# Optimization experiments

Hardware: AMD Instinct MI355X
Metric: run time of the kernel (lower is better)

Reference implementation:

```python
import jax, jax.numpy as jnp
import numpy as np

B = 256      # graphs per batch
N = 512      # nodes per graph
FEAT = 64    # num_features
H = 64       # nhid
DEG = 16     # avg degree
RATIO = 0.5  # pooling_ratio
E = B * N * DEG


def setup_inputs() -> dict:
    key = jax.random.key(0)
    ks = jax.random.split(key, 12)
    # edges constructed within each graph via offsets
    src_loc = jax.random.randint(ks[0], (B, N * DEG), 0, N)
    dst_loc = jax.random.randint(ks[1], (B, N * DEG), 0, N)
    offs = (jnp.arange(B) * N)[:, None]
    edge_src = (src_loc + offs).reshape(-1).astype(jnp.int32)
    edge_dst = (dst_loc + offs).reshape(-1).astype(jnp.int32)
    batch = jnp.repeat(jnp.arange(B, dtype=jnp.int32), N)
    x = jax.random.normal(ks[2], (B * N, FEAT), dtype=jnp.float32)
    edge_attr = jax.random.uniform(ks[3], (E,), dtype=jnp.float32) + 0.1
    s1 = 1.0 / np.sqrt(FEAT)
    s2 = 1.0 / np.sqrt(H)
    return {
        "x": x,
        "edge_attr": edge_attr,
        "W1": jax.random.normal(ks[4], (FEAT, H), jnp.float32) * s1,
        "b1": jnp.zeros((H,), jnp.float32),
        "Wp1": jax.random.normal(ks[5], (H, 1), jnp.float32) * s2,
        "bp1": jnp.zeros((1,), jnp.float32),
        "W2": jax.random.normal(ks[6], (H, H), jnp.float32) * s2,
        "b2": jnp.zeros((H,), jnp.float32),
        "Wp2": jax.random.normal(ks[7], (H, 1), jnp.float32) * s2,
        "bp2": jnp.zeros((1,), jnp.float32),
        "edge_src": edge_src,
        "edge_dst": edge_dst,
        "batch": batch,
    }


def gcn_conv(x, W, b, src, dst, ew, n):
    """PyG GCNConv: sym-normalized weighted adjacency + self-loops (weight 1)."""
    h = x @ W                                   # [n, out]
    deg = jnp.zeros((n,), x.dtype).at[dst].add(ew) + 1.0  # self-loop adds 1
    dinv = jax.lax.rsqrt(deg)
    coef = dinv[dst] * ew * dinv[src]           # [E]
    out = jnp.zeros_like(h).at[dst].add(coef[:, None] * h[src])
    out = out + h * (1.0 / deg)[:, None]        # self-loop term: deg^-0.5 * 1 * deg^-0.5
    return out + b


def sag_pool(x, src, dst, ew, Wp, bp, n_per):
    """SAGPool: score = GCNConv(x)->1, per-graph top-k, gate by tanh(score),
    filter edges (dropped edges represented by zero weight)."""
    n = x.shape[0]
    score = gcn_conv(x, Wp, bp, src, dst, ew, n)[:, 0]   # [n]
    k = int(np.ceil(RATIO * n_per))
    _, idx = jax.lax.top_k(score.reshape(B, n_per), k)   # [B, k] local indices
    perm = (idx + (jnp.arange(B) * n_per)[:, None]).reshape(-1)
    xn = x[perm] * jnp.tanh(score[perm])[:, None]        # [B*k, H]
    newid = jnp.full((n,), -1, jnp.int32).at[perm].set(
        jnp.arange(B * k, dtype=jnp.int32))
    ns, nd = newid[src], newid[dst]
    valid = (ns >= 0) & (nd >= 0)
    ew2 = jnp.where(valid, ew, 0.0)
    ns = jnp.where(valid, ns, 0)
    nd = jnp.where(valid, nd, 0)
    return xn, ns, nd, ew2, k


def readout(x, k):
    """[gmp || gap] per graph; each graph has exactly k nodes, contiguous."""
    xg = x.reshape(B, k, -1)
    return jnp.concatenate([xg.max(axis=1), xg.mean(axis=1)], axis=1)  # [B, 2H]


def reference(x, edge_attr, W1, b1, Wp1, bp1, W2, b2, Wp2, bp2,
              edge_src, edge_dst, batch):
    n0 = x.shape[0]
    h = jax.nn.relu(gcn_conv(x, W1, b1, edge_src, edge_dst, edge_attr, n0))
    h, s1, d1, w1e, k1 = sag_pool(h, edge_src, edge_dst, edge_attr, Wp1, bp1, N)
    x1 = readout(h, k1)
    h = jax.nn.relu(gcn_conv(h, W2, b2, s1, d1, w1e, B * k1))
    h, _, _, _, k2 = sag_pool(h, s1, d1, w1e, Wp2, bp2, k1)
    x2 = readout(h, k2)
    return (x1 + x2) / 2.0
```

## Files before the change

kernel.cpp:

```cpp
#include <hip/hip_runtime.h>
#include <math.h>

#define BG   256
#define NN   512
#define EPG  (NN * 16)
#define NE   (BG * EPG)
#define N0   (BG * NN)
#define K1   256
#define N1_  (BG * K1)
#define K2   128
#define N2_  (BG * K2)

__device__ __forceinline__ float4 f4fma(float s, float4 a, float4 c) {
    c.x = fmaf(s, a.x, c.x); c.y = fmaf(s, a.y, c.y);
    c.z = fmaf(s, a.z, c.z); c.w = fmaf(s, a.w, c.w);
    return c;
}

template <int NPG, bool REMAP>
__global__ __launch_bounds__(512)
void stage_head_kernel(const int* __restrict__ esrc, const int* __restrict__ edst,
                       const float* __restrict__ eatt, const int* __restrict__ nid,
                       int2* __restrict__ pairs, int* __restrict__ rowstart,
                       int* __restrict__ rowcnt, float* __restrict__ dinv,
                       const float4* __restrict__ X4, const float4* __restrict__ W4,
                       float4* __restrict__ Y4, int nrows, int mmb) {
    __shared__ __align__(16) char smem[52224];
    if ((int)blockIdx.x < BG) {
        int2*  lpair = (int2*)smem;
        int*   cnt   = (int*)(smem + 32768);
        float* wsum  = (float*)(smem + 32768) + NPG;
        int*   scn   = (int*)(smem + 32768) + 2 * NPG;
        float* sdinv = (float*)(smem + 32768) + 3 * NPG;
        int*   wtot  = (int*)(smem + 32768) + 4 * NPG;
        int g = blockIdx.x;
        int e0 = g * EPG, nbase = g * NPG;
        for (int ii = threadIdx.x; ii < NPG; ii += 512) { cnt[ii] = 0; wsum[ii] = 0.f; }
        __syncthreads();
        const int4*   edst4 = (const int4*)(edst + e0);
        const int4*   esrc4 = (const int4*)(esrc + e0);
        const float4* eatt4 = (const float4*)(eatt + e0);
        int ed[16]; int es[16]; float ea[16];
#pragma unroll
        for (int c = 0; c < 4; ++c) {
            int ch = threadIdx.x + c * 512;
            int4   dd = edst4[ch];
            int4   ss = esrc4[ch];
            float4 ww = eatt4[ch];
            ed[c * 4 + 0] = dd.x; ed[c * 4 + 1] = dd.y; ed[c * 4 + 2] = dd.z; ed[c * 4 + 3] = dd.w;
            es[c * 4 + 0] = ss.x; es[c * 4 + 1] = ss.y; es[c * 4 + 2] = ss.z; es[c * 4 + 3] = ss.w;
            ea[c * 4 + 0] = ww.x; ea[c * 4 + 1] = ww.y; ea[c * 4 + 2] = ww.z; ea[c * 4 + 3] = ww.w;
        }
        if (REMAP) {
#pragma unroll
            for (int j = 0; j < 16; ++j) { ed[j] = nid[ed[j]]; es[j] = nid[es[j]]; }
        }
#pragma unroll
        for (int j = 0; j < 16; ++j) {
            bool valid = !REMAP || (ed[j] >= 0 && es[j] >= 0);
            if (valid) {
                int dl = ed[j] - nbase;
                atomicAdd(&cnt[dl], 1);
                atomicAdd(&wsum[dl], ea[j]);
            }
        }
        __syncthreads();
        int i = threadIdx.x;
        int lane = i & 63, wvid = i >> 6;
        int xval = (i < NPG) ? cnt[i] : 0;
        int xs = xval;
#pragma unroll
        for (int off = 1; off < 64; off <<= 1) {
            int v = __shfl_up(xs, off, 64);
            if (lane >= off) xs += v;
        }
        if (lane == 63) wtot[wvid] = xs;
        __syncthreads();
        int woff = 0, total = 0;
#pragma unroll
        for (int t = 0; t < 8; ++t) {
            int wt = wtot[t];
            if (t < wvid) woff += wt;
            total += wt;
        }
        xs += woff;
        if (i < NPG) {
            int st = xs - xval;
            rowstart[nbase + i] = e0 + st;
            rowcnt[nbase + i]   = xval;
            float di = rsqrtf(wsum[i] + 1.0f);
            dinv[nbase + i] = di;
            sdinv[i] = di;
            scn[i] = st;
        }
        __syncthreads();
        int slots[16]; float cf[16];
#pragma unroll
        for (int j = 0; j < 16; ++j) {
            bool valid = !REMAP || (ed[j] >= 0 && es[j] >= 0);
            slots[j] = -1;
            if (valid) {
                int dl = ed[j] - nbase, sl = es[j] - nbase;
                cf[j] = sdinv[dl] * ea[j] * sdinv[sl];
                slots[j] = atomicAdd(&scn[dl], 1);
            }
        }
#pragma unroll
        for (int j = 0; j < 16; ++j)
            if (slots[j] >= 0 && slots[j] < 4096)
                lpair[slots[j]] = make_int2(es[j], __float_as_int(cf[j]));
        __syncthreads();
        int n0 = total < 4096 ? total : 4096;
        for (int k = threadIdx.x; k < n0; k += 512) pairs[e0 + k] = lpair[k];
        __syncthreads();
        if (total > 4096) {
#pragma unroll
            for (int j = 0; j < 16; ++j)
                if (slots[j] >= 4096)
                    lpair[slots[j] - 4096] = make_int2(es[j], __float_as_int(cf[j]));
            __syncthreads();
            int n1 = total - 4096;
            for (int k = threadIdx.x; k < n1; k += 512) pairs[e0 + 4096 + k] = lpair[k];
        }
    } else {
        float (*sW)[68] = (float (*)[68])smem;
        int p = threadIdx.x >> 8;
        int t = threadIdx.x & 255;
        float (*sX)[68] = (float (*)[68])(smem + 17408 + p * 17408);
#pragma unroll
        for (int u = 0; u < 2; ++u) {
            int idx = threadIdx.x + u * 512;
            int r = idx >> 4, c4 = idx & 15;
            *(float4*)&sW[r][c4 * 4] = W4[idx];
        }
        int mb = blockIdx.x - BG;
        int ntiles = nrows >> 6;
        int rg = t >> 4, cg = t & 15;
        for (int tile = mb * 2 + p; tile < ntiles; tile += mmb * 2) {
            __syncthreads();
            int row0 = tile << 6;
#pragma unroll
            for (int u = 0; u < 4; ++u) {
                int idx = t + u * 256;
                int r = idx >> 4, c4 = idx & 15;
                *(float4*)&sX[r][c4 * 4] = X4[(size_t)(row0 + r) * 16 + c4];
            }
            __syncthreads();
            float4 acc0 = make_float4(0.f, 0.f, 0.f, 0.f);
            float4 acc1 = acc0, acc2 = acc0, acc3 = acc0;
#pragma unroll
            for (int k4 = 0; k4 < 16; ++k4) {
                float4 xv0 = *(const float4*)&sX[rg * 4 + 0][k4 * 4];
                float4 xv1 = *(const float4*)&sX[rg * 4 + 1][k4 * 4];
                float4 xv2 = *(const float4*)&sX[rg * 4 + 2][k4 * 4];
                float4 xv3 = *(const float4*)&sX[rg * 4 + 3][k4 * 4];
                float4 wv0 = *(const float4*)&sW[k4 * 4 + 0][cg * 4];
                float4 wv1 = *(const float4*)&sW[k4 * 4 + 1][cg * 4];
                float4 wv2 = *(const float4*)&sW[k4 * 4 + 2][cg * 4];
                float4 wv3 = *(const float4*)&sW[k4 * 4 + 3][cg * 4];
                acc0 = f4fma(xv0.x, wv0, acc0); acc0 = f4fma(xv0.y, wv1, acc0);
                acc0 = f4fma(xv0.z, wv2, acc0); acc0 = f4fma(xv0.w, wv3, acc0);
                acc1 = f4fma(xv1.x, wv0, acc1); acc1 = f4fma(xv1.y, wv1, acc1);
                acc1 = f4fma(xv1.z, wv2, acc1); acc1 = f4fma(xv1.w, wv3, acc1);
                acc2 = f4fma(xv2.x, wv0, acc2); acc2 = f4fma(xv2.y, wv1, acc2);
                acc2 = f4fma(xv2.z, wv2, acc2); acc2 = f4fma(xv2.w, wv3, acc2);
                acc3 = f4fma(xv3.x, wv0, acc3); acc3 = f4fma(xv3.y, wv1, acc3);
                acc3 = f4fma(xv3.z, wv2, acc3); acc3 = f4fma(xv3.w, wv3, acc3);
            }
            size_t ob = (size_t)(row0 + rg * 4) * 16 + cg;
            Y4[ob]      = acc0;
            Y4[ob + 16] = acc1;
            Y4[ob + 32] = acc2;
            Y4[ob + 48] = acc3;
        }
    }
}

template <int NPG, int K, bool FINAL>
__global__ __launch_bounds__(512)
void tail_kernel(const float4* __restrict__ hx4, const int2* __restrict__ pairs,
                 const int* __restrict__ rowstart, const int* __restrict__ rowcnt,
                 const float* __restrict__ dinv, const float4* __restrict__ b4,
                 const float4* __restrict__ wp4, const float* __restrict__ bp,
                 int* __restrict__ nid, float4* __restrict__ xn4,
                 float* __restrict__ xr, const float* __restrict__ x1r,
                 float* __restrict__ out) {
    constexpr int PASSES = NPG / 32;
    __shared__ __align__(16) char smem[NPG * 68 * 4];
    float* shx = (float*)smem;
    float* shp = (float*)smem;
    float* ssc = (float*)smem + NPG;
    int*   rnk = (int*)smem + 2 * NPG;
    float4* smx = (float4*)(smem + 3 * NPG * 4);
    float4* ssm = smx + 32 * 16;

    int g = blockIdx.x, nbase = g * NPG;
    int t = threadIdx.x;
    int lane16 = t & 15, sub = (t >> 4) & 3, wv = t >> 6;
    for (int i = t; i < NPG * 16; i += 512) {
        int r = i >> 4, c4 = i & 15;
        *(float4*)&shx[r * 68 + c4 * 4] = hx4[(size_t)nbase * 16 + i];
    }
    __syncthreads();
    float4 acc[PASSES];
    float  hpreg[PASSES];
    float4 bb = b4[lane16];
    float4 w4 = wp4[lane16];
#pragma unroll
    for (int p = 0; p < PASSES; ++p) {
        int nl = p * 32 + wv * 4 + sub;
        int node = nbase + nl;
        float di = dinv[node];
        int st = rowstart[node], cn = rowcnt[node];
        float dii = di * di;
        float4 a = *(const float4*)&shx[nl * 68 + lane16 * 4];
        a.x = fmaf(a.x, dii, bb.x);
        a.y = fmaf(a.y, dii, bb.y);
        a.z = fmaf(a.z, dii, bb.z);
        a.w = fmaf(a.w, dii, bb.w);
        for (int j = 0; j < cn; ++j) {
            int2 pr = pairs[st + j];
            const float4 v = *(const float4*)&shx[(pr.x - nbase) * 68 + lane16 * 4];
            a = f4fma(__int_as_float(pr.y), v, a);
        }
        a.x = fmaxf(a.x, 0.f); a.y = fmaxf(a.y, 0.f);
        a.z = fmaxf(a.z, 0.f); a.w = fmaxf(a.w, 0.f);
        acc[p] = a;
        float tt = a.x * w4.x + a.y * w4.y + a.z * w4.z + a.w * w4.w;
        tt += __shfl_xor(tt, 1, 64); tt += __shfl_xor(tt, 2, 64);
        tt += __shfl_xor(tt, 4, 64); tt += __shfl_xor(tt, 8, 64);
        hpreg[p] = tt;
    }
    __syncthreads();
#pragma unroll
    for (int p = 0; p < PASSES; ++p) {
        int nl = p * 32 + wv * 4 + sub;
        if (lane16 == 0) shp[nl] = hpreg[p];
    }
    __syncthreads();
    for (int i = t; i < NPG; i += 512) {
        int st = rowstart[nbase + i], cn = rowcnt[nbase + i];
        float di = dinv[nbase + i];
        float a = fmaf(shp[i], di * di, bp[0]);
        for (int j = 0; j < cn; ++j) {
            int2 pr = pairs[st + j];
            a = fmaf(__int_as_float(pr.y), shp[pr.x - nbase], a);
        }
        ssc[i] = a;
    }
    __syncthreads();
    for (int i = t; i < NPG; i += 512) {
        float si = ssc[i];
        int rank = 0;
        for (int j = 0; j < NPG; ++j) {
            float sj = ssc[j];
            rank += (sj > si) || (sj == si && j < i);
        }
        rnk[i] = rank;
        if (!FINAL) nid[nbase + i] = (rank < K) ? (g * K + rank) : -1;
    }
    __syncthreads();
    float4 mx = make_float4(-3.402823466e38f, -3.402823466e38f, -3.402823466e38f, -3.402823466e38f);
    float4 sm = make_float4(0.f, 0.f, 0.f, 0.f);
#pragma unroll
    for (int p = 0; p < PASSES; ++p) {
        int nl = p * 32 + wv * 4 + sub;
        int r = rnk[nl];
        if (r < K) {
            float gt = tanhf(ssc[nl]);
            float4 v = acc[p];
            v.x *= gt; v.y *= gt; v.z *= gt; v.w *= gt;
            if (!FINAL) xn4[((size_t)g * K + r) * 16 + lane16] = v;
            mx.x = fmaxf(mx.x, v.x); mx.y = fmaxf(mx.y, v.y);
            mx.z = fmaxf(mx.z, v.z); mx.w = fmaxf(mx.w, v.w);
            sm.x += v.x; sm.y += v.y; sm.z += v.z; sm.w += v.w;
        }
    }
    int grp = t >> 4;
    smx[grp * 16 + lane16] = mx;
    ssm[grp * 16 + lane16] = sm;
    __syncthreads();
    if (grp == 0) {
#pragma unroll
        for (int u = 1; u < 32; ++u) {
            float4 a = smx[u * 16 + lane16], b = ssm[u * 16 + lane16];
            mx.x = fmaxf(mx.x, a.x); mx.y = fmaxf(mx.y, a.y);
            mx.z = fmaxf(mx.z, a.z); mx.w = fmaxf(mx.w, a.w);
            sm.x += b.x; sm.y += b.y; sm.z += b.z; sm.w += b.w;
        }
        float invK = 1.f / K;
        int c = lane16 * 4;
        float mr[4] = {mx.x, mx.y, mx.z, mx.w};
        float ar[4] = {sm.x * invK, sm.y * invK, sm.z * invK, sm.w * invK};
#pragma unroll
        for (int u = 0; u < 4; ++u) {
            if (FINAL) {
                out[g * 128 + c + u]      = 0.5f * (x1r[g * 128 + c + u]      + mr[u]);
                out[g * 128 + 64 + c + u] = 0.5f * (x1r[g * 128 + 64 + c + u] + ar[u]);
            } else {
                xr[g * 128 + c + u]      = mr[u];
                xr[g * 128 + 64 + c + u] = ar[u];
            }
        }
    }
}

extern "C" void kernel_launch(void* const* d_in, const int* in_sizes, int n_in,
                              void* d_out, int out_size, void* d_ws, size_t ws_size,
                              hipStream_t stream) {
    const float* x    = (const float*)d_in[0];
    const float* eatt = (const float*)d_in[1];
    const float* W1   = (const float*)d_in[2];
    const float* b1   = (const float*)d_in[3];
    const float* Wp1  = (const float*)d_in[4];
    const float* bp1  = (const float*)d_in[5];
    const float* W2   = (const float*)d_in[6];
    const float* b2   = (const float*)d_in[7];
    const float* Wp2  = (const float*)d_in[8];
    const float* bp2  = (const float*)d_in[9];
    const int*   esrc = (const int*)d_in[10];
    const int*   edst = (const int*)d_in[11];
    float* out = (float*)d_out;

    float* ws = (float*)d_ws;
    size_t o = 0;
    float* A    = ws + o; o += (size_t)N0 * 64;
    float* xn1  = ws + o; o += (size_t)N1_ * 64;
    int2*  prs  = (int2*)(ws + o); o += (size_t)NE * 2;
    int*   rst  = (int*)(ws + o); o += N0;
    int*   rcn  = (int*)(ws + o); o += N0;
    float* dinv = ws + o; o += N0;
    int*   nid  = (int*)(ws + o); o += N0;
    float* x1r  = ws + o; o += BG * 128;

    float* hx1 = A;
    float* hx2 = A;

    stage_head_kernel<NN, false><<<BG + 512, 512, 0, stream>>>(
        esrc, edst, eatt, nullptr, prs, rst, rcn, dinv,
        (const float4*)x, (const float4*)W1, (float4*)hx1, N0, 512);
    tail_kernel<NN, K1, false><<<BG, 512, 0, stream>>>(
        (const float4*)hx1, prs, rst, rcn, dinv, (const float4*)b1,
        (const float4*)Wp1, bp1, nid, (float4*)xn1, x1r, nullptr, nullptr);
    stage_head_kernel<K1, true><<<BG + 256, 512, 0, stream>>>(
        esrc, edst, eatt, nid, prs, rst, rcn, dinv,
        (const float4*)xn1, (const float4*)W2, (float4*)hx2, N1_, 256);
    tail_kernel<K1, K2, true><<<BG, 512, 0, stream>>>(
        (const float4*)hx2, prs, rst, rcn, dinv, (const float4*)b2,
        (const float4*)Wp2, bp2, nullptr, nullptr, nullptr, x1r, out);
}
```

Measured before the change: 247.2 us.

## Sort nodes by degree and aggregate full feature rows per thread in tail

The tail kernel now buckets nodes by in-degree with a shared-memory histogram and prefix scan, then assigns one node per thread so each thread accumulates all 64 features for its row. The aim is to cut wavefront divergence from uneven neighbour counts and to reuse each loaded pair across 16 float4s, with a one-ahead prefetch of the next pair. Pair sources are stored as graph-local indices so the subtraction of nbase is dropped in the inner loops. In exchange it uses 64 accumulator registers per thread, more shared memory and extra barriers, and leaves half the threads idle when NPG is 256; the per-thread row reads from shared memory may also cause bank conflicts.

```diff
diff --git a/kernel.cpp b/kernel.cpp
--- a/kernel.cpp
+++ b/kernel.cpp
@@ -108,7 +108,7 @@
 #pragma unroll
         for (int j = 0; j < 16; ++j)
             if (slots[j] >= 0 && slots[j] < 4096)
-                lpair[slots[j]] = make_int2(es[j], __float_as_int(cf[j]));
+                lpair[slots[j]] = make_int2(es[j] - nbase, __float_as_int(cf[j]));
         __syncthreads();
         int n0 = total < 4096 ? total : 4096;
         for (int k = threadIdx.x; k < n0; k += 512) pairs[e0 + k] = lpair[k];
@@ -117,7 +117,7 @@
 #pragma unroll
             for (int j = 0; j < 16; ++j)
                 if (slots[j] >= 4096)
-                    lpair[slots[j] - 4096] = make_int2(es[j], __float_as_int(cf[j]));
+                    lpair[slots[j] - 4096] = make_int2(es[j] - nbase, __float_as_int(cf[j]));
             __syncthreads();
             int n1 = total - 4096;
             for (int k = threadIdx.x; k < n1; k += 512) pairs[e0 + 4096 + k] = lpair[k];
@@ -186,65 +186,107 @@
                  float* __restrict__ xr, const float* __restrict__ x1r,
                  float* __restrict__ out) {
     constexpr int PASSES = NPG / 32;
-    __shared__ __align__(16) char smem[NPG * 68 * 4];
-    float* shx = (float*)smem;
-    float* shp = (float*)smem;
-    float* ssc = (float*)smem + NPG;
-    int*   rnk = (int*)smem + 2 * NPG;
-    float4* smx = (float4*)(smem + 3 * NPG * 4);
-    float4* ssm = smx + 32 * 16;
+    constexpr int SH_A  = NPG * 68;
+    constexpr int SH_UN = 4096;
+    __shared__ __align__(16) float smem[SH_A + SH_UN + 2 * NPG + 64 + 64];
+    float*  shx  = smem;
+    int*    perm = (int*)(smem + SH_A);
+    float*  shp  = smem + SH_A + NPG;
+    float4* smx  = (float4*)(smem + SH_A);
+    float4* ssm  = (float4*)(smem + SH_A + 2048);
+    float*  ssc  = smem + SH_A + SH_UN;
+    int*    rnk  = (int*)(smem + SH_A + SH_UN + NPG);
+    float*  sbw  = smem + SH_A + SH_UN + 2 * NPG;
+    int*    hist = (int*)(smem + SH_A + SH_UN + 2 * NPG + 64);
 
     int g = blockIdx.x, nbase = g * NPG;
     int t = threadIdx.x;
-    int lane16 = t & 15, sub = (t >> 4) & 3, wv = t >> 6;
+    int lane16 = t & 15, sub = (t >> 4) & 3, wv = t >> 6, lane = t & 63;
+
     for (int i = t; i < NPG * 16; i += 512) {
         int r = i >> 4, c4 = i & 15;
         *(float4*)&shx[r * 68 + c4 * 4] = hx4[(size_t)nbase * 16 + i];
     }
-    __syncthreads();
-    float4 acc[PASSES];
-    float  hpreg[PASSES];
-    float4 bb = b4[lane16];
+    if (t < 64) { sbw[t] = ((const float*)b4)[t]; hist[t] = 0; }
+    __syncthreads();
+    for (int i = t; i < NPG; i += 512) {
+        int c = min(rowcnt[nbase + i], 63);
+        atomicAdd(&hist[c], 1);
+    }
+    __syncthreads();
+    if (t < 64) {
+        int v = hist[t], s = v;
+#pragma unroll
+        for (int off = 1; off < 64; off <<= 1) {
+            int u = __shfl_up(s, off, 64);
+            if (lane >= off) s += u;
+        }
+        hist[t] = s - v;
+    }
+    __syncthreads();
+    for (int i = t; i < NPG; i += 512) {
+        int c = min(rowcnt[nbase + i], 63);
+        int pos = atomicAdd(&hist[c], 1);
+        perm[pos] = i;
+    }
+    __syncthreads();
+    int idx = wv * 64 + lane;
+    float4 acc[16];
+    int nl = 0;
+    if (idx < NPG) {
+        nl = perm[idx];
+        int st = rowstart[nbase + nl], cn = rowcnt[nbase + nl];
+        float di = dinv[nbase + nl], dii = di * di;
+#pragma unroll
+        for (int c = 0; c < 16; ++c) {
+            float4 xv = *(const float4*)&shx[nl * 68 + c * 4];
+            acc[c].x = fmaf(xv.x, dii, sbw[c * 4 + 0]);
+            acc[c].y = fmaf(xv.y, dii, sbw[c * 4 + 1]);
+            acc[c].z = fmaf(xv.z, dii, sbw[c * 4 + 2]);
+            acc[c].w = fmaf(xv.w, dii, sbw[c * 4 + 3]);
+        }
+        int2 pc = (cn > 0) ? pairs[st] : make_int2(0, 0);
+        for (int j = 0; j < cn; ++j) {
+            int2 pn = (j + 1 < cn) ? pairs[st + j + 1] : make_int2(0, 0);
+            float cf = __int_as_float(pc.y);
+            int   s  = pc.x;
+#pragma unroll
+            for (int c = 0; c < 16; ++c)
+                acc[c] = f4fma(cf, *(const float4*)&shx[s * 68 + c * 4], acc[c]);
+            pc = pn;
+        }
+#pragma unroll
+        for (int c = 0; c < 16; ++c) {
+            acc[c].x = fmaxf(acc[c].x, 0.f); acc[c].y = fmaxf(acc[c].y, 0.f);
+            acc[c].z = fmaxf(acc[c].z, 0.f); acc[c].w = fmaxf(acc[c].w, 0.f);
+        }
+    }
+    __syncthreads();
+    if (idx < NPG) {
+#pragma unroll
+        for (int c = 0; c < 16; ++c)
+            *(float4*)&shx[nl * 68 + c * 4] = acc[c];
+    }
+    __syncthreads();
     float4 w4 = wp4[lane16];
 #pragma unroll
     for (int p = 0; p < PASSES; ++p) {
-        int nl = p * 32 + wv * 4 + sub;
-        int node = nbase + nl;
-        float di = dinv[node];
-        int st = rowstart[node], cn = rowcnt[node];
-        float dii = di * di;
-        float4 a = *(const float4*)&shx[nl * 68 + lane16 * 4];
-        a.x = fmaf(a.x, dii, bb.x);
-        a.y = fmaf(a.y, dii, bb.y);
-        a.z = fmaf(a.z, dii, bb.z);
-        a.w = fmaf(a.w, dii, bb.w);
-        for (int j = 0; j < cn; ++j) {
-            int2 pr = pairs[st + j];
-            const float4 v = *(const float4*)&shx[(pr.x - nbase) * 68 + lane16 * 4];
-            a = f4fma(__int_as_float(pr.y), v, a);
-        }
-        a.x = fmaxf(a.x, 0.f); a.y = fmaxf(a.y, 0.f);
-        a.z = fmaxf(a.z, 0.f); a.w = fmaxf(a.w, 0.f);
-        acc[p] = a;
+        int n2 = p * 32 + wv * 4 + sub;
+        float4 a = *(const float4*)&shx[n2 * 68 + lane16 * 4];
         float tt = a.x * w4.x + a.y * w4.y + a.z * w4.z + a.w * w4.w;
         tt += __shfl_xor(tt, 1, 64); tt += __shfl_xor(tt, 2, 64);
         tt += __shfl_xor(tt, 4, 64); tt += __shfl_xor(tt, 8, 64);
-        hpreg[p] = tt;
-    }
-    __syncthreads();
-#pragma unroll
-    for (int p = 0; p < PASSES; ++p) {
-        int nl = p * 32 + wv * 4 + sub;
-        if (lane16 == 0) shp[nl] = hpreg[p];
-    }
-    __syncthreads();
-    for (int i = t; i < NPG; i += 512) {
+        if (lane16 == 0) shp[n2] = tt;
+    }
+    __syncthreads();
+    if (t < NPG) {
+        int i = perm[t];
         int st = rowstart[nbase + i], cn = rowcnt[nbase + i];
         float di = dinv[nbase + i];
         float a = fmaf(shp[i], di * di, bp[0]);
         for (int j = 0; j < cn; ++j) {
             int2 pr = pairs[st + j];
-            a = fmaf(__int_as_float(pr.y), shp[pr.x - nbase], a);
+            a = fmaf(__int_as_float(pr.y), shp[pr.x], a);
         }
         ssc[i] = a;
     }
@@ -264,11 +306,11 @@
     float4 sm = make_float4(0.f, 0.f, 0.f, 0.f);
 #pragma unroll
     for (int p = 0; p < PASSES; ++p) {
-        int nl = p * 32 + wv * 4 + sub;
-        int r = rnk[nl];
+        int n2 = p * 32 + wv * 4 + sub;
+        int r = rnk[n2];
         if (r < K) {
-            float gt = tanhf(ssc[nl]);
-            float4 v = acc[p];
+            float gt = tanhf(ssc[n2]);
+            float4 v = *(const float4*)&shx[n2 * 68 + lane16 * 4];
             v.x *= gt; v.y *= gt; v.z *= gt; v.w *= gt;
             if (!FINAL) xn4[((size_t)g * K + r) * 16 + lane16] = v;
             mx.x = fmaxf(mx.x, v.x); mx.y = fmaxf(mx.y, v.y);
@@ -277,6 +319,7 @@
         }
     }
     int grp = t >> 4;
+    __syncthreads();
     smx[grp * 16 + lane16] = mx;
     ssm[grp * 16 + lane16] = sm;
     __syncthreads();
```

New measurement: 226.2 us. -8.5%, faster.
